# Performance work log

Measured on AMD Instinct MI355X. Metric: run time of the kernel, lower is better.

The kernel has to match this reference:

```python
import jax, jax.numpy as jnp
import numpy as np

NUM_GROUPS = 32
EPS = 1e-6


def group_norm(x, gamma, beta):
    # x: [B, C, H, W]
    b, c, h, w = x.shape
    xg = x.reshape(b, NUM_GROUPS, c // NUM_GROUPS, h, w)
    mean = xg.mean(axis=(2, 3, 4), keepdims=True)
    var = xg.var(axis=(2, 3, 4), keepdims=True)
    xn = ((xg - mean) * jax.lax.rsqrt(var + EPS)).reshape(b, c, h, w)
    return xn * gamma[None, :, None, None] + beta[None, :, None, None]


def setup_inputs() -> dict:
    key = jax.random.key(0)
    ks = jax.random.split(key, 10)
    B, C, H, W = 2, 512, 64, 64
    s = 1.0 / np.sqrt(C)
    return {
        "x": jax.random.normal(ks[0], (B, C, H, W), dtype=jnp.float32),
        "gamma": jnp.ones((C,), jnp.float32),
        "beta": jnp.zeros((C,), jnp.float32),
        "Wq": jax.random.normal(ks[1], (C, C), jnp.float32) * s,
        "bq": jnp.zeros((C,), jnp.float32),
        "Wk": jax.random.normal(ks[2], (C, C), jnp.float32) * s,
        "bk": jnp.zeros((C,), jnp.float32),
        "Wv": jax.random.normal(ks[3], (C, C), jnp.float32) * s,
        "bv": jnp.zeros((C,), jnp.float32),
        "Wo": jax.random.normal(ks[4], (C, C), jnp.float32) * s,
        "bo": jnp.zeros((C,), jnp.float32),
    }


def reference(x, gamma, beta, Wq, bq, Wk, bk, Wv, bv, Wo, bo):
    b, c, h, w = x.shape
    hn = group_norm(x, gamma, beta)               # [B,C,H,W]
    hf = hn.reshape(b, c, h * w)                  # [B,C,N]
    # 1x1 convs == channel matmuls
    q = jnp.einsum('oc,bcn->bon', Wq, hf) + bq[None, :, None]
    k = jnp.einsum('oc,bcn->bon', Wk, hf) + bk[None, :, None]
    v = jnp.einsum('oc,bcn->bon', Wv, hf) + bv[None, :, None]
    scale = float(c) ** -0.5
    scores = jnp.einsum('bci,bcj->bij', q, k) * scale   # [B,N,N]
    attn = jax.nn.softmax(scores, axis=-1)
    out = jnp.einsum('bij,bcj->bci', attn, v)            # [B,C,N]
    out = jnp.einsum('oc,bcn->bon', Wo, out) + bo[None, :, None]
    return x + out.reshape(b, c, h, w)
```

## Files before the change

### kernel.cpp

```cpp
#include <hip/hip_runtime.h>

#define BB 2
#define CC 512
#define NS 4096
#define NGROUP 32
#define TILE 128
#define RSTRIDE 132

typedef __bf16 bf16_8 __attribute__((ext_vector_type(8)));
typedef __bf16 bf16_4 __attribute__((ext_vector_type(4)));
typedef float f32_4 __attribute__((ext_vector_type(4)));

#define SMEM_BYTES 33792

__device__ __forceinline__ void gld_lds16(const __bf16* g, __bf16* l) {
  __builtin_amdgcn_global_load_lds(
      (const __attribute__((address_space(1))) unsigned int*)g,
      (__attribute__((address_space(3))) unsigned int*)l, 16, 0, 0);
}

__global__ __launch_bounds__(256) void gn_stats(const float* __restrict__ x,
                                                float* __restrict__ stats) {
  const float4* p = (const float4*)(x + (size_t)blockIdx.x * 65536);
  float s = 0.f, q = 0.f;
  for (int i = threadIdx.x; i < 16384; i += 256) {
    float4 v = p[i];
    s += v.x + v.y + v.z + v.w;
    q += v.x * v.x + v.y * v.y + v.z * v.z + v.w * v.w;
  }
#pragma unroll
  for (int off = 32; off > 0; off >>= 1) {
    s += __shfl_down(s, off, 64);
    q += __shfl_down(q, off, 64);
  }
  __shared__ float ls[4], lq[4];
  int wave = threadIdx.x >> 6, lane = threadIdx.x & 63;
  if (lane == 0) { ls[wave] = s; lq[wave] = q; }
  __syncthreads();
  if (threadIdx.x == 0) {
    float S = ls[0] + ls[1] + ls[2] + ls[3];
    float Q = lq[0] + lq[1] + lq[2] + lq[3];
    float mean = S * (1.f / 65536.f);
    float var = Q * (1.f / 65536.f) - mean * mean;
    stats[blockIdx.x * 2] = mean;
    stats[blockIdx.x * 2 + 1] = rsqrtf(var + 1e-6f);
  }
}

__global__ __launch_bounds__(256) void gn_apply_t(const float* __restrict__ x,
                                                  const float* __restrict__ stats,
                                                  const float* __restrict__ gamma,
                                                  const float* __restrict__ beta,
                                                  __bf16* __restrict__ hnT) {
  __shared__ float tile[32][33];
  int b = blockIdx.z;
  int c0 = blockIdx.y * 32;
  int n0 = blockIdx.x * 32;
  int tx = threadIdx.x;
  int ty = threadIdx.y;
  const float* xb = x + (size_t)b * CC * NS;
#pragma unroll
  for (int i = 0; i < 4; i++) {
    int c = c0 + ty + i * 8;
    float mean = stats[(b * NGROUP + (c >> 4)) * 2 + 0];
    float rstd = stats[(b * NGROUP + (c >> 4)) * 2 + 1];
    float v = xb[(size_t)c * NS + n0 + tx];
    tile[ty + i * 8][tx] = (v - mean) * rstd * gamma[c] + beta[c];
  }
  __syncthreads();
  __bf16* out = hnT + (size_t)b * NS * CC;
#pragma unroll
  for (int i = 0; i < 4; i++) {
    int n = n0 + ty + i * 8;
    out[(size_t)n * CC + c0 + tx] = (__bf16)tile[tx][ty + i * 8];
  }
}

__global__ __launch_bounds__(256) void cvt_w(const float* __restrict__ w0, const float* __restrict__ w1,
                                             const float* __restrict__ w2, const float* __restrict__ w3,
                                             __bf16* __restrict__ o0, __bf16* __restrict__ o1,
                                             __bf16* __restrict__ o2, __bf16* __restrict__ o3) {
  int tsel = blockIdx.x >> 8;
  int i = (blockIdx.x & 255) * 256 + threadIdx.x;
  const float* src = tsel == 0 ? w0 : tsel == 1 ? w1 : tsel == 2 ? w2 : w3;
  __bf16* dst = tsel == 0 ? o0 : tsel == 1 ? o1 : tsel == 2 ? o2 : o3;
  float4 v = ((const float4*)src)[i];
  bf16_4 r;
  r[0] = (__bf16)v.x; r[1] = (__bf16)v.y; r[2] = (__bf16)v.z; r[3] = (__bf16)v.w;
  ((bf16_4*)dst)[i] = r;
}

__device__ __forceinline__ void gemm_core(const __bf16* __restrict__ A, const __bf16* __restrict__ B,
                                          int K, int lda, int ldb,
                                          __bf16* lA, __bf16* lB, f32_4 (&acc)[4][4]) {
  const int t = threadIdx.x;
  const int lane = t & 63;
  const int wave = t >> 6;
  const int lrow = lane & 15, quad = lane >> 4;
  const int wrow = (wave >> 1) * 64, wcol = (wave & 1) * 64;
  const int co = (quad ^ ((lrow >> 1) & 3)) * 8;
  const int r0 = t >> 2;
  const int kp = ((t & 3) ^ ((t >> 3) & 3)) * 8;
  const __bf16* pA0 = A + (size_t)r0 * lda + kp;
  const __bf16* pA1 = A + (size_t)(r0 + 64) * lda + kp;
  const __bf16* pB0 = B + (size_t)r0 * ldb + kp;
  const __bf16* pB1 = B + (size_t)(r0 + 64) * ldb + kp;
  for (int k0 = 0; k0 < K; k0 += 64) {
    __syncthreads();
    gld_lds16(pA0 + k0,      &lA[t * 8]);
    gld_lds16(pA1 + k0,      &lA[2048 + t * 8]);
    gld_lds16(pA0 + k0 + 32, &lA[4096 + t * 8]);
    gld_lds16(pA1 + k0 + 32, &lA[6144 + t * 8]);
    gld_lds16(pB0 + k0,      &lB[t * 8]);
    gld_lds16(pB1 + k0,      &lB[2048 + t * 8]);
    gld_lds16(pB0 + k0 + 32, &lB[4096 + t * 8]);
    gld_lds16(pB1 + k0 + 32, &lB[6144 + t * 8]);
    __syncthreads();
#pragma unroll
    for (int ks = 0; ks < 2; ks++) {
      const __bf16* la = lA + ks * 4096;
      const __bf16* lb = lB + ks * 4096;
      bf16_8 af[4], bfr[4];
#pragma unroll
      for (int i = 0; i < 4; i++)
        af[i] = *(const bf16_8*)&la[(wrow + i * 16 + lrow) * 32 + co];
#pragma unroll
      for (int j = 0; j < 4; j++)
        bfr[j] = *(const bf16_8*)&lb[(wcol + j * 16 + lrow) * 32 + co];
#pragma unroll
      for (int i = 0; i < 4; i++)
#pragma unroll
        for (int j = 0; j < 4; j++)
          acc[i][j] = __builtin_amdgcn_mfma_f32_16x16x32_bf16(af[i], bfr[j], acc[i][j], 0, 0, 0);
    }
  }
}

__device__ __forceinline__ void stage_acc(float* ls, const f32_4 (&acc)[4][4], int pass) {
  const int t = threadIdx.x;
  const int lane = t & 63, wave = t >> 6;
  const int lrow = lane & 15, quad = lane >> 4;
  const int wrow = (wave >> 1) * 64, wcol = (wave & 1) * 64;
  if ((wrow >> 6) == pass) {
#pragma unroll
    for (int i = 0; i < 4; i++)
#pragma unroll
      for (int r = 0; r < 4; r++)
#pragma unroll
        for (int jj = 0; jj < 4; jj++)
          ls[(i * 16 + quad * 4 + r) * RSTRIDE + wcol + jj * 16 + lrow] = acc[i][jj][r];
  }
}

__device__ __forceinline__ void drain_bf16(const float* ls, __bf16* gdst, int ldg) {
  const int t = threadIdx.x;
#pragma unroll
  for (int k2 = 0; k2 < 8; k2++) {
    int idx = k2 * 256 + t;
    int row = idx >> 5, col = (idx & 31) * 4;
    f32_4 v = *(const f32_4*)&ls[row * RSTRIDE + col];
    bf16_4 o;
    o[0] = (__bf16)v[0]; o[1] = (__bf16)v[1]; o[2] = (__bf16)v[2]; o[3] = (__bf16)v[3];
    *(bf16_4*)&gdst[(size_t)row * ldg + col] = o;
  }
}

__global__ __launch_bounds__(256) void qkv_gemm(const __bf16* __restrict__ hnT,
                                                const __bf16* __restrict__ Wq,
                                                const __bf16* __restrict__ Wk,
                                                const __bf16* __restrict__ Wv,
                                                const float* __restrict__ bq,
                                                const float* __restrict__ bk,
                                                const float* __restrict__ bv,
                                                __bf16* __restrict__ qT,
                                                __bf16* __restrict__ kT,
                                                __bf16* __restrict__ vv) {
  __shared__ char smem[SMEM_BYTES];
  __bf16* lA = (__bf16*)smem;
  __bf16* lB = (__bf16*)(smem + 16384);
  float* lsr = (float*)smem;
  const int b = blockIdx.z;
  const int id = blockIdx.x;
  const int sel = id >> 7;
  const int r = id & 127;
  const long long sBNC = (long long)NS * CC;
  const long long sBCN = (long long)CC * NS;

  int m0, n0, N;
  const __bf16 *Ap, *Bp;
  __bf16* Cp;
  const float* bias;
  if (sel < 2) {
    m0 = (r >> 2) * TILE;
    n0 = (r & 3) * TILE;
    Ap = hnT + (size_t)b * sBNC + (size_t)m0 * CC;
    Bp = (sel == 0 ? Wq : Wk) + (size_t)n0 * CC;
    Cp = (sel == 0 ? qT : kT) + (size_t)b * sBNC;
    bias = (sel == 0 ? bq : bk);
    N = CC;
  } else {
    m0 = (r & 3) * TILE;
    n0 = (r >> 2) * TILE;
    Ap = Wv + (size_t)m0 * CC;
    Bp = hnT + (size_t)b * sBNC + (size_t)n0 * CC;
    Cp = vv + (size_t)b * sBCN;
    bias = bv;
    N = NS;
  }

  f32_4 acc[4][4];
#pragma unroll
  for (int i = 0; i < 4; i++)
#pragma unroll
    for (int j = 0; j < 4; j++) acc[i][j] = {0.f, 0.f, 0.f, 0.f};

  gemm_core(Ap, Bp, CC, CC, CC, lA, lB, acc);

  const int t = threadIdx.x;
  const int lane = t & 63;
  const int lrow = lane & 15, quad = lane >> 4;
  const int wave = t >> 6;
  const int wrow = (wave >> 1) * 64, wcol = (wave & 1) * 64;
#pragma unroll
  for (int i = 0; i < 4; i++)
#pragma unroll
    for (int r2 = 0; r2 < 4; r2++) {
      float rowb = (sel == 2) ? bias[m0 + wrow + i * 16 + quad * 4 + r2] : 0.f;
#pragma unroll
      for (int j = 0; j < 4; j++) {
        float cb = (sel < 2) ? bias[n0 + wcol + j * 16 + lrow] : rowb;
        acc[i][j][r2] += cb;
      }
    }

#pragma unroll
  for (int p = 0; p < 2; p++) {
    __syncthreads();
    stage_acc(lsr, acc, p);
    __syncthreads();
    drain_bf16(lsr, Cp + (size_t)(m0 + p * 64) * N + n0, N);
  }
}

__global__ __launch_bounds__(256) void e_gemm(const __bf16* __restrict__ qT,
                                              const __bf16* __restrict__ kT,
                                              __bf16* __restrict__ E,
                                              float* __restrict__ l,
                                              float scale) {
  __shared__ char smem[32768];
  __bf16* lA = (__bf16*)smem;
  __bf16* lB = (__bf16*)(smem + 16384);
  const int g = blockIdx.x;
  const int j = g & 7;
  const int b = j & 1;
  const int moct = j >> 1;
  const int k = g >> 3;
  const int sc = k >> 6;
  const int rem = k & 63;
  const int m0 = (moct * 8 + (rem >> 3)) * TILE;
  const int n0 = (sc * 8 + (rem & 7)) * TILE;
  const long long sBNC = (long long)NS * CC;
  const long long sBNN = (long long)NS * NS;
  const __bf16* Ap = qT + (size_t)b * sBNC + (size_t)m0 * CC;
  const __bf16* Bp = kT + (size_t)b * sBNC + (size_t)n0 * CC;

  f32_4 acc[4][4];
#pragma unroll
  for (int i = 0; i < 4; i++)
#pragma unroll
    for (int jj = 0; jj < 4; jj++) acc[i][jj] = {0.f, 0.f, 0.f, 0.f};

  gemm_core(Ap, Bp, CC, CC, CC, lA, lB, acc);

  const int t = threadIdx.x;
  const int lane = t & 63;
  const int lrow = lane & 15, quad = lane >> 4;
  const int wave = t >> 6;
  const int wrow = (wave >> 1) * 64, wcol = (wave & 1) * 64;
  __bf16* Ep = E + (size_t)b * sBNN;
  float* lp = l + (size_t)b * NS;
#pragma unroll
  for (int i = 0; i < 4; i++) {
#pragma unroll
    for (int r = 0; r < 4; r++) {
      int gm = m0 + wrow + i * 16 + quad * 4 + r;
      float rp = 0.f;
#pragma unroll
      for (int jj = 0; jj < 4; jj++) {
        int gn = n0 + wcol + jj * 16 + lrow;
        float ev = __expf(acc[i][jj][r] * scale);
        rp += ev;
        Ep[(size_t)gm * NS + gn] = (__bf16)ev;
      }
      rp += __shfl_down(rp, 8, 16);
      rp += __shfl_down(rp, 4, 16);
      rp += __shfl_down(rp, 2, 16);
      rp += __shfl_down(rp, 1, 16);
      if (lrow == 0) atomicAdd(&lp[gm], rp);
    }
  }
}

__global__ __launch_bounds__(256) void ao_split4(const __bf16* __restrict__ E,
                                                 const __bf16* __restrict__ vv,
                                                 __bf16* __restrict__ p0,
                                                 __bf16* __restrict__ p1,
                                                 __bf16* __restrict__ p2,
                                                 __bf16* __restrict__ p3) {
  __shared__ char smem[SMEM_BYTES];
  __bf16* lA = (__bf16*)smem;
  __bf16* lB = (__bf16*)(smem + 16384);
  float* lsr = (float*)smem;
  const int g = blockIdx.x;
  const int j = g & 7;
  const int b = j & 1;
  const int split = j >> 1;
  const int k = g >> 3;
  const int m0 = (k >> 2) * TILE;
  const int n0 = (k & 3) * TILE;
  const long long sBNN = (long long)NS * NS;
  const long long sBCN = (long long)CC * NS;
  const long long sBNC = (long long)NS * CC;
  const __bf16* Ap = E + (size_t)b * sBNN + (size_t)m0 * NS + (size_t)split * 1024;
  const __bf16* Bp = vv + (size_t)b * sBCN + (size_t)n0 * NS + (size_t)split * 1024;
  __bf16* Cp = (split == 0 ? p0 : split == 1 ? p1 : split == 2 ? p2 : p3) + (size_t)b * sBNC;

  f32_4 acc[4][4];
#pragma unroll
  for (int i = 0; i < 4; i++)
#pragma unroll
    for (int jj = 0; jj < 4; jj++) acc[i][jj] = {0.f, 0.f, 0.f, 0.f};

  gemm_core(Ap, Bp, 1024, NS, NS, lA, lB, acc);

#pragma unroll
  for (int p = 0; p < 2; p++) {
    __syncthreads();
    stage_acc(lsr, acc, p);
    __syncthreads();
    drain_bf16(lsr, Cp + (size_t)(m0 + p * 64) * CC + n0, CC);
  }
}

__global__ __launch_bounds__(256) void reduce_ao4(const __bf16* __restrict__ p0,
                                                  const __bf16* __restrict__ p1,
                                                  const __bf16* __restrict__ p2,
                                                  const __bf16* __restrict__ p3,
                                                  const float* __restrict__ l,
                                                  __bf16* __restrict__ o) {
  int i = blockIdx.x * 256 + threadIdx.x;
  int row = i >> 6;
  float inv = 1.f / l[row];
  bf16_8 a = ((const bf16_8*)p0)[i];
  bf16_8 c = ((const bf16_8*)p1)[i];
  bf16_8 d = ((const bf16_8*)p2)[i];
  bf16_8 e = ((const bf16_8*)p3)[i];
  bf16_8 r;
#pragma unroll
  for (int k = 0; k < 8; k++)
    r[k] = (__bf16)(((float)a[k] + (float)c[k] + (float)d[k] + (float)e[k]) * inv);
  ((bf16_8*)o)[i] = r;
}

__global__ __launch_bounds__(256) void wo_split(const __bf16* __restrict__ Wo,
                                               const __bf16* __restrict__ aoT,
                                               __bf16* __restrict__ pw0,
                                               __bf16* __restrict__ pw1) {
  __shared__ char smem[SMEM_BYTES];
  __bf16* lA = (__bf16*)smem;
  __bf16* lB = (__bf16*)(smem + 16384);
  float* lsr = (float*)smem;
  const int b = blockIdx.z & 1;
  const int split = blockIdx.z >> 1;
  const int m0 = blockIdx.y * TILE;
  const int n0 = blockIdx.x * TILE;
  const long long sBNC = (long long)NS * CC;
  const long long sBCN = (long long)CC * NS;
  const __bf16* Ap = Wo + (size_t)m0 * CC + (size_t)split * 256;
  const __bf16* Bp = aoT + (size_t)b * sBNC + (size_t)n0 * CC + (size_t)split * 256;
  __bf16* Cp = (split ? pw1 : pw0) + (size_t)b * sBCN;

  f32_4 acc[4][4];
#pragma unroll
  for (int i = 0; i < 4; i++)
#pragma unroll
    for (int j = 0; j < 4; j++) acc[i][j] = {0.f, 0.f, 0.f, 0.f};

  gemm_core(Ap, Bp, 256, CC, CC, lA, lB, acc);

#pragma unroll
  for (int p = 0; p < 2; p++) {
    __syncthreads();
    stage_acc(lsr, acc, p);
    __syncthreads();
    drain_bf16(lsr, Cp + (size_t)(m0 + p * 64) * NS + n0, NS);
  }
}

__global__ __launch_bounds__(256) void final_out(const __bf16* __restrict__ pw0,
                                                 const __bf16* __restrict__ pw1,
                                                 const float* __restrict__ bo,
                                                 const float* __restrict__ x,
                                                 float* __restrict__ out) {
  int i = blockIdx.x * 256 + threadIdx.x;
  int o = (i >> 10) & (CC - 1);
  float bias = bo[o];
  bf16_4 a = ((const bf16_4*)pw0)[i];
  bf16_4 c = ((const bf16_4*)pw1)[i];
  float4 xr = ((const float4*)x)[i];
  float4 r;
  r.x = (float)a[0] + (float)c[0] + bias + xr.x;
  r.y = (float)a[1] + (float)c[1] + bias + xr.y;
  r.z = (float)a[2] + (float)c[2] + bias + xr.z;
  r.w = (float)a[3] + (float)c[3] + bias + xr.w;
  ((float4*)out)[i] = r;
}

extern "C" void kernel_launch(void* const* d_in, const int* in_sizes, int n_in,
                              void* d_out, int out_size, void* d_ws, size_t ws_size,
                              hipStream_t stream) {
  const float* x = (const float*)d_in[0];
  const float* gamma = (const float*)d_in[1];
  const float* beta = (const float*)d_in[2];
  const float* Wq = (const float*)d_in[3];
  const float* bq = (const float*)d_in[4];
  const float* Wk = (const float*)d_in[5];
  const float* bk = (const float*)d_in[6];
  const float* Wv = (const float*)d_in[7];
  const float* bv = (const float*)d_in[8];
  const float* Wo = (const float*)d_in[9];
  const float* bo = (const float*)d_in[10];
  float* out = (float*)d_out;

  char* ws = (char*)d_ws;
  __bf16* hnT = (__bf16*)(ws + 0);
  __bf16* qT  = (__bf16*)(ws + 8388608);
  __bf16* kT  = (__bf16*)(ws + 16777216);
  __bf16* vv  = (__bf16*)(ws + 25165824);
  __bf16* aoT = (__bf16*)(ws + 33554432);
  __bf16* Eb  = (__bf16*)(ws + 41943040);
  __bf16* pw0 = (__bf16*)(ws + 41943040);
  __bf16* pw1 = (__bf16*)(ws + 50331648);
  __bf16* Wqb = (__bf16*)(ws + 109051904);
  __bf16* Wkb = (__bf16*)(ws + 109576192);
  __bf16* Wvb = (__bf16*)(ws + 110100480);
  __bf16* Wob = (__bf16*)(ws + 110624768);
  float* stats = (float*)(ws + 111149056);
  float* lsum = (float*)(ws + 109051904);
  __bf16* p0 = hnT;
  __bf16* p1 = qT;
  __bf16* p2 = kT;
  __bf16* p3 = aoT;

  const float scale = 0.044194173824159216f;

  cvt_w<<<1024, 256, 0, stream>>>(Wq, Wk, Wv, Wo, Wqb, Wkb, Wvb, Wob);
  gn_stats<<<BB * NGROUP, 256, 0, stream>>>(x, stats);
  gn_apply_t<<<dim3(NS / 32, CC / 32, BB), dim3(32, 8), 0, stream>>>(x, stats, gamma, beta, hnT);

  qkv_gemm<<<dim3(384, 1, BB), 256, 0, stream>>>(hnT, Wqb, Wkb, Wvb, bq, bk, bv, qT, kT, vv);

  hipMemsetAsync(lsum, 0, BB * NS * sizeof(float), stream);
  e_gemm<<<2048, 256, 0, stream>>>(qT, kT, Eb, lsum, scale);

  ao_split4<<<1024, 256, 0, stream>>>(Eb, vv, p0, p1, p2, p3);
  reduce_ao4<<<2048, 256, 0, stream>>>(p0, p1, p2, p3, lsum, aoT);

  wo_split<<<dim3(NS / TILE, CC / TILE, 2 * BB), 256, 0, stream>>>(Wob, aoT, pw0, pw1);
  final_out<<<4096, 256, 0, stream>>>(pw0, pw1, bo, x, out);
}
```

Baseline: 264.6 us.

## Use 8-wave 512-thread blocks for qkv, ao and wo GEMMs

Adds a GEMM core variant where eight waves share each 128x128 tile, with a 2x4 wave grid and 64x32 per wave, so each wave holds half the accumulators. Each thread now issues one global-to-LDS load per operand per K-half instead of two. The qkv, ao_split4 and wo_split kernels switch to 512-thread launches with matching staging and drain routines, aiming at more latency hiding and lower register pressure per wave. The trade-off is more barrier participants per block and fewer MFMAs per LDS fragment read, since the A fragments are reused across only two B fragments.

```diff
diff --git a/kernel.cpp b/kernel.cpp
--- a/kernel.cpp
+++ b/kernel.cpp
@@ -90,9 +90,78 @@
   ((bf16_4*)dst)[i] = r;
 }
 
-__device__ __forceinline__ void gemm_core(const __bf16* __restrict__ A, const __bf16* __restrict__ B,
-                                          int K, int lda, int ldb,
-                                          __bf16* lA, __bf16* lB, f32_4 (&acc)[4][4]) {
+__device__ __forceinline__ void gemm_core8(const __bf16* __restrict__ A, const __bf16* __restrict__ B,
+                                           int K, int lda, int ldb,
+                                           __bf16* lA, __bf16* lB, f32_4 (&acc)[4][2]) {
+  const int t = threadIdx.x;
+  const int lane = t & 63;
+  const int wave = t >> 6;
+  const int lrow = lane & 15, quad = lane >> 4;
+  const int wrow = (wave >> 2) * 64, wcol = (wave & 3) * 32;
+  const int co = (quad ^ ((lrow >> 1) & 3)) * 8;
+  const int r0 = t >> 2;
+  const int kp = ((t & 3) ^ ((t >> 3) & 3)) * 8;
+  const __bf16* pA = A + (size_t)r0 * lda + kp;
+  const __bf16* pB = B + (size_t)r0 * ldb + kp;
+  for (int k0 = 0; k0 < K; k0 += 64) {
+    __syncthreads();
+    gld_lds16(pA + k0,      &lA[t * 8]);
+    gld_lds16(pA + k0 + 32, &lA[4096 + t * 8]);
+    gld_lds16(pB + k0,      &lB[t * 8]);
+    gld_lds16(pB + k0 + 32, &lB[4096 + t * 8]);
+    __syncthreads();
+#pragma unroll
+    for (int ks = 0; ks < 2; ks++) {
+      const __bf16* la = lA + ks * 4096;
+      const __bf16* lb = lB + ks * 4096;
+      bf16_8 af[4], bfr[2];
+#pragma unroll
+      for (int i = 0; i < 4; i++)
+        af[i] = *(const bf16_8*)&la[(wrow + i * 16 + lrow) * 32 + co];
+#pragma unroll
+      for (int j = 0; j < 2; j++)
+        bfr[j] = *(const bf16_8*)&lb[(wcol + j * 16 + lrow) * 32 + co];
+#pragma unroll
+      for (int i = 0; i < 4; i++)
+#pragma unroll
+        for (int j = 0; j < 2; j++)
+          acc[i][j] = __builtin_amdgcn_mfma_f32_16x16x32_bf16(af[i], bfr[j], acc[i][j], 0, 0, 0);
+    }
+  }
+}
+
+__device__ __forceinline__ void stage_acc8(float* ls, const f32_4 (&acc)[4][2], int pass) {
+  const int t = threadIdx.x;
+  const int lane = t & 63, wave = t >> 6;
+  const int lrow = lane & 15, quad = lane >> 4;
+  const int wrow = (wave >> 2) * 64, wcol = (wave & 3) * 32;
+  if ((wrow >> 6) == pass) {
+#pragma unroll
+    for (int i = 0; i < 4; i++)
+#pragma unroll
+      for (int r = 0; r < 4; r++)
+#pragma unroll
+        for (int jj = 0; jj < 2; jj++)
+          ls[(i * 16 + quad * 4 + r) * RSTRIDE + wcol + jj * 16 + lrow] = acc[i][jj][r];
+  }
+}
+
+__device__ __forceinline__ void drain_bf16_8(const float* ls, __bf16* gdst, int ldg) {
+  const int t = threadIdx.x;
+#pragma unroll
+  for (int k2 = 0; k2 < 4; k2++) {
+    int idx = k2 * 512 + t;
+    int row = idx >> 5, col = (idx & 31) * 4;
+    f32_4 v = *(const f32_4*)&ls[row * RSTRIDE + col];
+    bf16_4 o;
+    o[0] = (__bf16)v[0]; o[1] = (__bf16)v[1]; o[2] = (__bf16)v[2]; o[3] = (__bf16)v[3];
+    *(bf16_4*)&gdst[(size_t)row * ldg + col] = o;
+  }
+}
+
+__device__ __forceinline__ void gemm_core4(const __bf16* __restrict__ A, const __bf16* __restrict__ B,
+                                           int K, int lda, int ldb,
+                                           __bf16* lA, __bf16* lB, f32_4 (&acc)[4][4]) {
   const int t = threadIdx.x;
   const int lane = t & 63;
   const int wave = t >> 6;
@@ -136,45 +205,16 @@
   }
 }
 
-__device__ __forceinline__ void stage_acc(float* ls, const f32_4 (&acc)[4][4], int pass) {
-  const int t = threadIdx.x;
-  const int lane = t & 63, wave = t >> 6;
-  const int lrow = lane & 15, quad = lane >> 4;
-  const int wrow = (wave >> 1) * 64, wcol = (wave & 1) * 64;
-  if ((wrow >> 6) == pass) {
-#pragma unroll
-    for (int i = 0; i < 4; i++)
-#pragma unroll
-      for (int r = 0; r < 4; r++)
-#pragma unroll
-        for (int jj = 0; jj < 4; jj++)
-          ls[(i * 16 + quad * 4 + r) * RSTRIDE + wcol + jj * 16 + lrow] = acc[i][jj][r];
-  }
-}
-
-__device__ __forceinline__ void drain_bf16(const float* ls, __bf16* gdst, int ldg) {
-  const int t = threadIdx.x;
-#pragma unroll
-  for (int k2 = 0; k2 < 8; k2++) {
-    int idx = k2 * 256 + t;
-    int row = idx >> 5, col = (idx & 31) * 4;
-    f32_4 v = *(const f32_4*)&ls[row * RSTRIDE + col];
-    bf16_4 o;
-    o[0] = (__bf16)v[0]; o[1] = (__bf16)v[1]; o[2] = (__bf16)v[2]; o[3] = (__bf16)v[3];
-    *(bf16_4*)&gdst[(size_t)row * ldg + col] = o;
-  }
-}
-
-__global__ __launch_bounds__(256) void qkv_gemm(const __bf16* __restrict__ hnT,
-                                                const __bf16* __restrict__ Wq,
-                                                const __bf16* __restrict__ Wk,
-                                                const __bf16* __restrict__ Wv,
-                                                const float* __restrict__ bq,
-                                                const float* __restrict__ bk,
-                                                const float* __restrict__ bv,
-                                                __bf16* __restrict__ qT,
-                                                __bf16* __restrict__ kT,
-                                                __bf16* __restrict__ vv) {
+__global__ __launch_bounds__(512, 4) void qkv_gemm(const __bf16* __restrict__ hnT,
+                                                   const __bf16* __restrict__ Wq,
+                                                   const __bf16* __restrict__ Wk,
+                                                   const __bf16* __restrict__ Wv,
+                                                   const float* __restrict__ bq,
+                                                   const float* __restrict__ bk,
+                                                   const float* __restrict__ bv,
+                                                   __bf16* __restrict__ qT,
+                                                   __bf16* __restrict__ kT,
+                                                   __bf16* __restrict__ vv) {
   __shared__ char smem[SMEM_BYTES];
   __bf16* lA = (__bf16*)smem;
   __bf16* lB = (__bf16*)(smem + 16384);
@@ -208,26 +248,26 @@
     N = NS;
   }
 
-  f32_4 acc[4][4];
+  f32_4 acc[4][2];
 #pragma unroll
   for (int i = 0; i < 4; i++)
 #pragma unroll
-    for (int j = 0; j < 4; j++) acc[i][j] = {0.f, 0.f, 0.f, 0.f};
-
-  gemm_core(Ap, Bp, CC, CC, CC, lA, lB, acc);
+    for (int j = 0; j < 2; j++) acc[i][j] = {0.f, 0.f, 0.f, 0.f};
+
+  gemm_core8(Ap, Bp, CC, CC, CC, lA, lB, acc);
 
   const int t = threadIdx.x;
   const int lane = t & 63;
   const int lrow = lane & 15, quad = lane >> 4;
   const int wave = t >> 6;
-  const int wrow = (wave >> 1) * 64, wcol = (wave & 1) * 64;
+  const int wrow = (wave >> 2) * 64, wcol = (wave & 3) * 32;
 #pragma unroll
   for (int i = 0; i < 4; i++)
 #pragma unroll
     for (int r2 = 0; r2 < 4; r2++) {
       float rowb = (sel == 2) ? bias[m0 + wrow + i * 16 + quad * 4 + r2] : 0.f;
 #pragma unroll
-      for (int j = 0; j < 4; j++) {
+      for (int j = 0; j < 2; j++) {
         float cb = (sel < 2) ? bias[n0 + wcol + j * 16 + lrow] : rowb;
         acc[i][j][r2] += cb;
       }
@@ -236,9 +276,9 @@
 #pragma unroll
   for (int p = 0; p < 2; p++) {
     __syncthreads();
-    stage_acc(lsr, acc, p);
-    __syncthreads();
-    drain_bf16(lsr, Cp + (size_t)(m0 + p * 64) * N + n0, N);
+    stage_acc8(lsr, acc, p);
+    __syncthreads();
+    drain_bf16_8(lsr, Cp + (size_t)(m0 + p * 64) * N + n0, N);
   }
 }
 
@@ -270,7 +310,7 @@
 #pragma unroll
     for (int jj = 0; jj < 4; jj++) acc[i][jj] = {0.f, 0.f, 0.f, 0.f};
 
-  gemm_core(Ap, Bp, CC, CC, CC, lA, lB, acc);
+  gemm_core4(Ap, Bp, CC, CC, CC, lA, lB, acc);
 
   const int t = threadIdx.x;
   const int lane = t & 63;
@@ -301,12 +341,12 @@
   }
 }
 
-__global__ __launch_bounds__(256) void ao_split4(const __bf16* __restrict__ E,
-                                                 const __bf16* __restrict__ vv,
-                                                 __bf16* __restrict__ p0,
-                                                 __bf16* __restrict__ p1,
-                                                 __bf16* __restrict__ p2,
-                                                 __bf16* __restrict__ p3) {
+__global__ __launch_bounds__(512, 4) void ao_split4(const __bf16* __restrict__ E,
+                                                    const __bf16* __restrict__ vv,
+                                                    __bf16* __restrict__ p0,
+                                                    __bf16* __restrict__ p1,
+                                                    __bf16* __restrict__ p2,
+                                                    __bf16* __restrict__ p3) {
   __shared__ char smem[SMEM_BYTES];
   __bf16* lA = (__bf16*)smem;
   __bf16* lB = (__bf16*)(smem + 16384);
@@ -325,20 +365,20 @@
   const __bf16* Bp = vv + (size_t)b * sBCN + (size_t)n0 * NS + (size_t)split * 1024;
   __bf16* Cp = (split == 0 ? p0 : split == 1 ? p1 : split == 2 ? p2 : p3) + (size_t)b * sBNC;
 
-  f32_4 acc[4][4];
+  f32_4 acc[4][2];
 #pragma unroll
   for (int i = 0; i < 4; i++)
 #pragma unroll
-    for (int jj = 0; jj < 4; jj++) acc[i][jj] = {0.f, 0.f, 0.f, 0.f};
-
-  gemm_core(Ap, Bp, 1024, NS, NS, lA, lB, acc);
+    for (int jj = 0; jj < 2; jj++) acc[i][jj] = {0.f, 0.f, 0.f, 0.f};
+
+  gemm_core8(Ap, Bp, 1024, NS, NS, lA, lB, acc);
 
 #pragma unroll
   for (int p = 0; p < 2; p++) {
     __syncthreads();
-    stage_acc(lsr, acc, p);
-    __syncthreads();
-    drain_bf16(lsr, Cp + (size_t)(m0 + p * 64) * CC + n0, CC);
+    stage_acc8(lsr, acc, p);
+    __syncthreads();
+    drain_bf16_8(lsr, Cp + (size_t)(m0 + p * 64) * CC + n0, CC);
   }
 }
 
@@ -362,10 +402,10 @@
   ((bf16_8*)o)[i] = r;
 }
 
-__global__ __launch_bounds__(256) void wo_split(const __bf16* __restrict__ Wo,
-                                               const __bf16* __restrict__ aoT,
-                                               __bf16* __restrict__ pw0,
-                                               __bf16* __restrict__ pw1) {
+__global__ __launch_bounds__(512, 4) void wo_split(const __bf16* __restrict__ Wo,
+                                                   const __bf16* __restrict__ aoT,
+                                                   __bf16* __restrict__ pw0,
+                                                   __bf16* __restrict__ pw1) {
   __shared__ char smem[SMEM_BYTES];
   __bf16* lA = (__bf16*)smem;
   __bf16* lB = (__bf16*)(smem + 16384);
@@ -380,20 +420,20 @@
   const __bf16* Bp = aoT + (size_t)b * sBNC + (size_t)n0 * CC + (size_t)split * 256;
   __bf16* Cp = (split ? pw1 : pw0) + (size_t)b * sBCN;
 
-  f32_4 acc[4][4];
+  f32_4 acc[4][2];
 #pragma unroll
   for (int i = 0; i < 4; i++)
 #pragma unroll
-    for (int j = 0; j < 4; j++) acc[i][j] = {0.f, 0.f, 0.f, 0.f};
-
-  gemm_core(Ap, Bp, 256, CC, CC, lA, lB, acc);
+    for (int j = 0; j < 2; j++) acc[i][j] = {0.f, 0.f, 0.f, 0.f};
+
+  gemm_core8(Ap, Bp, 256, CC, CC, lA, lB, acc);
 
 #pragma unroll
   for (int p = 0; p < 2; p++) {
     __syncthreads();
-    stage_acc(lsr, acc, p);
-    __syncthreads();
-    drain_bf16(lsr, Cp + (size_t)(m0 + p * 64) * NS + n0, NS);
+    stage_acc8(lsr, acc, p);
+    __syncthreads();
+    drain_bf16_8(lsr, Cp + (size_t)(m0 + p * 64) * NS + n0, NS);
   }
 }
 
@@ -458,14 +498,14 @@
   gn_stats<<<BB * NGROUP, 256, 0, stream>>>(x, stats);
   gn_apply_t<<<dim3(NS / 32, CC / 32, BB), dim3(32, 8), 0, stream>>>(x, stats, gamma, beta, hnT);
 
-  qkv_gemm<<<dim3(384, 1, BB), 256, 0, stream>>>(hnT, Wqb, Wkb, Wvb, bq, bk, bv, qT, kT, vv);
+  qkv_gemm<<<dim3(384, 1, BB), 512, 0, stream>>>(hnT, Wqb, Wkb, Wvb, bq, bk, bv, qT, kT, vv);
 
   hipMemsetAsync(lsum, 0, BB * NS * sizeof(float), stream);
   e_gemm<<<2048, 256, 0, stream>>>(qT, kT, Eb, lsum, scale);
 
-  ao_split4<<<1024, 256, 0, stream>>>(Eb, vv, p0, p1, p2, p3);
+  ao_split4<<<1024, 512, 0, stream>>>(Eb, vv, p0, p1, p2, p3);
   reduce_ao4<<<2048, 256, 0, stream>>>(p0, p1, p2, p3, lsum, aoT);
 
-  wo_split<<<dim3(NS / TILE, CC / TILE, 2 * BB), 256, 0, stream>>>(Wob, aoT, pw0, pw1);
+  wo_split<<<dim3(NS / TILE, CC / TILE, 2 * BB), 512, 0, stream>>>(Wob, aoT, pw0, pw1);
   final_out<<<4096, 256, 0, stream>>>(pw0, pw1, bo, x, out);
 }
```

Result: faster. 258.3 us (-2.4%).
